# Optimization experiments

Hardware: AMD Instinct MI355X
Metric: run time of the kernel (lower is better)

The kernel has to match this reference:

```python
import jax, jax.numpy as jnp
import numpy as np

WAY, SHOT, P, FDIM, HDIM, NHEADS = 5, 5, 10, 640, 512, 8
H = W = 14
NUM_SPT = WAY * SHOT
EPS_BN = 1e-5
EPS_LN = 1e-5


def _l2norm(x, axis=-1):
    n = jnp.linalg.norm(x, axis=axis, keepdims=True)
    return x / jnp.maximum(n, 1e-12)


def _cbr(x, Wc, bc, g, beta):
    # 1x1 conv + BatchNorm(train stats) + ReLU. x: [N,C,H,W], Wc: [O,C]
    y = jnp.einsum('nchw,oc->nohw', x, Wc) + bc[None, :, None, None]
    mu = y.mean((0, 2, 3))
    var = y.var((0, 2, 3))
    y = (y - mu[None, :, None, None]) / jnp.sqrt(var[None, :, None, None] + EPS_BN)
    y = y * g[None, :, None, None] + beta[None, :, None, None]
    return jax.nn.relu(y)


def _mha(x, Wq, bq, Wk, bk, Wv, bv, Wa, ba, ln_g, ln_b):
    B, S, D = x.shape
    dk = D // NHEADS
    def proj(Wt, bt):
        return (x @ Wt.T + bt).reshape(B, S, NHEADS, dk).transpose(0, 2, 1, 3)
    q, k, v = proj(Wq, bq), proj(Wk, bk), proj(Wv, bv)
    scores = jnp.einsum('bhqd,bhkd->bhqk', q, k) / jnp.sqrt(jnp.asarray(dk, x.dtype))
    att = jax.nn.softmax(scores, axis=-1)
    ctx = jnp.einsum('bhqk,bhkd->bhqd', att, v).transpose(0, 2, 1, 3).reshape(B, S, D)
    out = ctx @ Wa.T + ba + x  # residual
    mu = out.mean(-1, keepdims=True)
    var = out.var(-1, keepdims=True)
    return ((out - mu) / jnp.sqrt(var + EPS_LN)) * ln_g + ln_b


def setup_inputs() -> dict:
    k = jax.random.key(0)
    ks = jax.random.split(k, 16)
    s = 0.02
    return {
        'key':   jax.random.normal(ks[0], (NUM_SPT + 75, FDIM, H, W), jnp.float32),
        'query': jax.random.normal(ks[1], (75, FDIM, H, W), jnp.float32),
        'Wc':  jax.random.normal(ks[2], (HDIM, FDIM), jnp.float32) * s,
        'bc':  jnp.zeros((HDIM,), jnp.float32),
        'g1':  jnp.ones((HDIM,), jnp.float32),
        'b1':  jnp.zeros((HDIM,), jnp.float32),
        'Wq':  jax.random.normal(ks[3], (HDIM, HDIM), jnp.float32) * s,
        'bq':  jnp.zeros((HDIM,), jnp.float32),
        'Wk':  jax.random.normal(ks[4], (HDIM, HDIM), jnp.float32) * s,
        'bk':  jnp.zeros((HDIM,), jnp.float32),
        'Wv':  jax.random.normal(ks[5], (HDIM, HDIM), jnp.float32) * s,
        'bv':  jnp.zeros((HDIM,), jnp.float32),
        'Wa':  jax.random.normal(ks[6], (HDIM, HDIM), jnp.float32) * s,
        'ba':  jnp.zeros((HDIM,), jnp.float32),
        'ln_g': jnp.ones((HDIM,), jnp.float32),
        'ln_b': jnp.zeros((HDIM,), jnp.float32),
        'Wm':  jax.random.normal(ks[7], (P, HDIM), jnp.float32) * s,
        'Wo':  jax.random.normal(ks[8], (FDIM, HDIM), jnp.float32) * s,
        'bo':  jnp.zeros((FDIM,), jnp.float32),
        'g2':  jnp.ones((FDIM,), jnp.float32),
        'b2':  jnp.zeros((FDIM,), jnp.float32),
    }


def reference(key, query, Wc, bc, g1, b1, Wq, bq, Wk, bk, Wv, bv, Wa, ba, ln_g, ln_b, Wm, Wo, bo, g2, b2):
    # proto_concept: conv1x1 + BN + ReLU
    key_ = _cbr(key, Wc, bc, g1, b1)                 # [B, HDIM, H, W]
    B, D, h, w = key_.shape
    feats = key_.transpose(0, 2, 3, 1).reshape(B, h * w, D)
    support = feats[:NUM_SPT].reshape(SHOT, WAY, h * w, D).mean(0)   # [WAY, hw, D]
    qf = feats[NUM_SPT:]                                             # [NQ, hw, D]
    nq = B - NUM_SPT

    support = _mha(support, Wq, bq, Wk, bk, Wv, bv, Wa, ba, ln_g, ln_b)
    qf = _mha(qf, Wq, bq, Wk, bk, Wv, bv, Wa, ba, ln_g, ln_b)

    # prototype formation: softmax over all support positions (dim 0)
    mw = (support @ Wm.T).reshape(-1, P, 1)          # [WAY*hw, P, 1]
    mw = jax.nn.softmax(mw, axis=0)
    sflat = support.reshape(-1, D)                   # [WAY*hw, D]
    protos = (mw * sflat[:, None, :]).sum(0)         # [P, D]

    # ---- query_loss (training branch) ----
    protos_n = _l2norm(protos)                       # [P, D]

    # diversity loss (faithful to original incl. triu over (P, D) dims)
    diff2 = (protos_n[None, :, :] - protos_n[:, None, :]) ** 2   # [P, P, D]
    dis = 1.0 - diff2[None]                                      # [1, P, P, D]
    dis = dis * (dis > 0).astype(dis.dtype)
    tri = jnp.triu(jnp.ones((P, D), dis.dtype), k=1)
    dis = dis * tri
    dis_loss = (dis.sum(1).sum(1) * 2.0 / (P * (P - 1))).mean()

    cst_loss = ((protos_n[1:] - protos_n[:-1]) ** 2).sum(-1).mean()

    # dual-softmax scoring (protos shared across batch)
    score = jnp.einsum('bnd,md->bnm', qf, protos_n)  # [NQ, hw, P]
    sp = jax.nn.softmax(score, axis=-1)
    new_q = _l2norm(jnp.einsum('bnm,md->bnd', sp, protos_n))

    idx = jnp.argmax(score, axis=-1)                 # top-1 proto per position
    pos = protos_n[idx]                              # [NQ, hw, D]
    fea_loss = jnp.mean((qf - pos) ** 2)

    uq = new_q.transpose(0, 2, 1).reshape(nq, D, h, w)
    updated = _cbr(uq, Wo, bo, g2, b2) + query       # [NQ, FDIM, H, W]
    return (updated, fea_loss, cst_loss, dis_loss)
```

## Files before the change

kernel.cpp:

```cpp
#include <hip/hip_runtime.h>
#include <math.h>

#define WAYS 5
#define SHOTS 5
#define PP 10
#define FDIMC 640
#define HD 512
#define SEQ 196
#define NB 100
#define NQB 75
#define NMHA 80
#define M1 (NB*SEQ)
#define MMHA (NMHA*SEQ)
#define MQ (NQB*SEQ)
#define NBLK_ROWK (MQ/4)
#define OUT_UPD (NQB*FDIMC*SEQ)

#define OFF_CS1S 0
#define OFF_CS1Q 512
#define OFF_CS2S 1024
#define OFF_CS2Q 1664
#define ZERO_FLOATS 2306
#define OFF_ST1SC 2308
#define OFF_ST1SH 2820
#define OFF_ST2SC 3332
#define OFF_ST2SH 3972
#define OFF_M    4612
#define OFF_PN   14412

#define RB 20480
#define RC (RB + 15439360)
#define RD (RC + 8028160)
#define RE (RD + 8028160)
#define RF (RE + 8028160)
#define RG (RF + 4014080)
#define RH (RG + 4014080)
#define OFF_XOUT (RB + 10000000)
#define OFF_FEAP (RF + 3763200)
#define OFF_WSM  RG
#define OFF_PPART (RG + 16384)

typedef __bf16 bf16x8 __attribute__((ext_vector_type(8)));
typedef float f32x4 __attribute__((ext_vector_type(4)));

__device__ __forceinline__ ushort f2bf(float f) {
  unsigned u = __float_as_uint(f);
  return (ushort)((u + 0x7fffu + ((u >> 16) & 1u)) >> 16);
}
__device__ __forceinline__ float bf2f(ushort u) {
  return __uint_as_float(((unsigned)u) << 16);
}

__device__ __forceinline__ f32x4 mfma16(bf16x8 a, bf16x8 b, f32x4 c) {
  return __builtin_amdgcn_mfma_f32_16x16x32_bf16(a, b, c, 0, 0, 0);
}

__device__ __forceinline__ float waveSum(float v) {
#pragma unroll
  for (int o = 32; o; o >>= 1) v += __shfl_xor(v, o, 64);
  return v;
}

__device__ __forceinline__ void gld16(const void* g, void* l) {
  __builtin_amdgcn_global_load_lds(
      (const __attribute__((address_space(1))) void*)g,
      (__attribute__((address_space(3))) void*)l,
      16, 0, 0);
}


__global__ __launch_bounds__(256) void key_transpose(const float* __restrict__ key,
                                                     ushort* __restrict__ keyT) {
  __shared__ float T[32][33];
  const int n = blockIdx.z, c0 = blockIdx.y*32, s0 = blockIdx.x*32;
  const int tj = threadIdx.x & 31, ti = threadIdx.x >> 5;
#pragma unroll
  for (int it = 0; it < 4; ++it) {
    const int cl = it*8 + ti;
    const int s = s0 + tj;
    T[cl][tj] = (s < SEQ) ? key[((size_t)n*FDIMC + c0 + cl)*SEQ + s] : 0.f;
  }
  __syncthreads();
#pragma unroll
  for (int it = 0; it < 4; ++it) {
    const int sl = it*8 + ti;
    const int s = s0 + sl;
    if (s < SEQ) keyT[((size_t)(n*SEQ + s))*FDIMC + c0 + tj] = f2bf(T[tj][sl]);
  }
}

__global__ void wconvert(const float* __restrict__ Wc, const float* __restrict__ Wq,
                         const float* __restrict__ Wk, const float* __restrict__ Wv,
                         const float* __restrict__ Wa, const float* __restrict__ Wo,
                         ushort* __restrict__ wh) {
  const int i = blockIdx.x*256 + threadIdx.x;
  float v;
  if (i < 327680) v = Wc[i];
  else if (i < 589824) v = Wq[i - 327680];
  else if (i < 851968) v = Wk[i - 589824];
  else if (i < 1114112) v = Wv[i - 851968];
  else if (i < 1376256) v = Wa[i - 1114112];
  else v = Wo[i - 1376256];
  wh[i] = f2bf(v);
}

template<int OM, int CS>
__global__ __launch_bounds__(256) void gemm_bf(const ushort* __restrict__ A,
    const ushort* __restrict__ W, const float* __restrict__ bias,
    float* __restrict__ Cf, ushort* __restrict__ Ch, int M, int N, int K,
    float* __restrict__ gsum, float* __restrict__ gsq) {
  __shared__ ushort As[128*32];
  __shared__ ushort Bs[128*32];
  __shared__ float csum[128], csq[128];
  const int tid = threadIdx.x;

  const int nwg = gridDim.x * gridDim.y;
  int flat = blockIdx.y * gridDim.x + blockIdx.x;
  {
    const int q = nwg >> 3, r = nwg & 7;
    const int j = flat & 7, t = flat >> 3;
    flat = (j < r ? j*(q+1) : r*(q+1) + (j-r)*q) + t;
  }
  const int m0 = (flat / gridDim.x) * 128;
  const int n0 = (flat % gridDim.x) * 128;

  const int w = tid >> 6, lane = tid & 63;
  const int wr = w >> 1, wc = w & 1;
  const int g = lane >> 4, c = lane & 15;

  const int srow = w*16 + (lane >> 2);
  const int sk   = (lane & 3) * 8;
  int ar0 = m0 + srow;       if (ar0 > M-1) ar0 = M-1;
  int ar1 = m0 + 64 + srow;  if (ar1 > M-1) ar1 = M-1;
  const ushort* Ap0 = A + (size_t)ar0*K + sk;
  const ushort* Ap1 = A + (size_t)ar1*K + sk;
  const ushort* Bp0 = W + (size_t)(n0 + srow)*K + sk;
  const ushort* Bp1 = W + (size_t)(n0 + 64 + srow)*K + sk;
  ushort* lA0 = &As[w*512];
  ushort* lA1 = &As[(4+w)*512];
  ushort* lB0 = &Bs[w*512];
  ushort* lB1 = &Bs[(4+w)*512];

  f32x4 acc[4][4];
#pragma unroll
  for (int i = 0; i < 4; ++i)
#pragma unroll
    for (int j = 0; j < 4; ++j) acc[i][j] = (f32x4)(0.0f);

  for (int k0 = 0; k0 < K; k0 += 32) {
    __syncthreads();
    gld16(Ap0 + k0, lA0);
    gld16(Ap1 + k0, lA1);
    gld16(Bp0 + k0, lB0);
    gld16(Bp1 + k0, lB1);
    __syncthreads();
    bf16x8 af[4], bfr[4];
#pragma unroll
    for (int mi = 0; mi < 4; ++mi)
      af[mi] = *(const bf16x8*)(&As[(wr*64 + mi*16 + c)*32 + g*8]);
#pragma unroll
    for (int ni = 0; ni < 4; ++ni)
      bfr[ni] = *(const bf16x8*)(&Bs[(wc*64 + ni*16 + c)*32 + g*8]);
#pragma unroll
    for (int mi = 0; mi < 4; ++mi)
#pragma unroll
      for (int ni = 0; ni < 4; ++ni)
        acc[mi][ni] = mfma16(af[mi], bfr[ni], acc[mi][ni]);
  }

  if (CS) {
    __syncthreads();
    if (tid < 128) { csum[tid] = 0.f; csq[tid] = 0.f; }
    __syncthreads();
  }

#pragma unroll
  for (int ni = 0; ni < 4; ++ni) {
    const int col = n0 + wc*64 + ni*16 + c;
    const float bb = bias[col];
    float ls = 0.f, lq = 0.f;
#pragma unroll
    for (int mi = 0; mi < 4; ++mi) {
#pragma unroll
      for (int q = 0; q < 4; ++q) {
        const int row = m0 + wr*64 + mi*16 + g*4 + q;
        if (row < M) {
          const float v = acc[mi][ni][q] + bb;
          if (OM == 0) Cf[(size_t)row*N + col] = v;
          else if (OM == 1) Ch[(size_t)row*N + col] = f2bf(v);
          else Ch[(size_t)row*N + col] = f2bf(v*0.125f);
          if (CS) { ls += v; lq += v*v; }
        }
      }
    }
    if (CS) {
      const int lcol = wc*64 + ni*16 + c;
      atomicAdd(&csum[lcol], ls);
      atomicAdd(&csq[lcol], lq);
    }
  }
  if (CS) {
    __syncthreads();
    if (tid < 128) {
      atomicAdd(&gsum[n0 + tid], csum[tid]);
      atomicAdd(&gsq[n0 + tid], csq[tid]);
    }
  }
}


__global__ void bn_finalize(const float* __restrict__ sums, const float* __restrict__ sumsq,
    const float* __restrict__ g, const float* __restrict__ b, int C, float invM,
    float* __restrict__ scale, float* __restrict__ shift) {
  const int c = blockIdx.x*256 + threadIdx.x;
  if (c >= C) return;
  const float mu = sums[c]*invM;
  const float var = sumsq[c]*invM - mu*mu;
  const float sc = rsqrtf(var + 1e-5f) * g[c];
  scale[c] = sc;
  shift[c] = b[c] - mu*sc;
}

__global__ __launch_bounds__(256) void bn1_apply(const ushort* __restrict__ y1,
    const float* __restrict__ scale, const float* __restrict__ shift,
    ushort* __restrict__ srawh, ushort* __restrict__ xbufh) {
  const int i8 = blockIdx.x*256 + threadIdx.x;
  if (i8 >= M1*HD/8) return;
  const int e = i8 << 3;
  const int col = e & (HD - 1);
  const uint4 raw = ((const uint4*)y1)[i8];
  unsigned rw[4] = {raw.x, raw.y, raw.z, raw.w};
  unsigned res[4];
#pragma unroll
  for (int j = 0; j < 4; ++j) {
    float v0 = bf2f((ushort)(rw[j] & 0xffffu));
    float v1 = bf2f((ushort)(rw[j] >> 16));
    v0 = fmaxf(fmaf(v0, scale[col + 2*j],     shift[col + 2*j]),     0.f);
    v1 = fmaxf(fmaf(v1, scale[col + 2*j + 1], shift[col + 2*j + 1]), 0.f);
    res[j] = (unsigned)f2bf(v0) | ((unsigned)f2bf(v1) << 16);
  }
  const uint4 o = make_uint4(res[0], res[1], res[2], res[3]);
  if (e < 25*SEQ*HD) ((uint4*)srawh)[i8] = o;
  else ((uint4*)xbufh)[i8 - (20*SEQ*HD/8)] = o;
}

__global__ void support_mean(const ushort* __restrict__ srawh, ushort* __restrict__ xbufh) {
  const int i8 = blockIdx.x*256 + threadIdx.x;
  if (i8 >= WAYS*SEQ*HD/8) return;
  const int e = i8 << 3;
  const int w = e / (SEQ*HD);
  const int rem = e - w*(SEQ*HD);
  float acc[8] = {};
#pragma unroll
  for (int s = 0; s < SHOTS; ++s) {
    const uint4 v = *(const uint4*)(srawh + (size_t)(s*WAYS + w)*(SEQ*HD) + rem);
    const unsigned rw[4] = {v.x, v.y, v.z, v.w};
#pragma unroll
    for (int j = 0; j < 4; ++j) {
      acc[2*j]   += bf2f((ushort)(rw[j] & 0xffffu));
      acc[2*j+1] += bf2f((ushort)(rw[j] >> 16));
    }
  }
  unsigned res[4];
#pragma unroll
  for (int j = 0; j < 4; ++j)
    res[j] = (unsigned)f2bf(acc[2*j]*0.2f) | ((unsigned)f2bf(acc[2*j+1]*0.2f) << 16);
  ((uint4*)xbufh)[i8] = make_uint4(res[0], res[1], res[2], res[3]);
}


__global__ __launch_bounds__(256) void attn_qk(const ushort* __restrict__ qb,
    const ushort* __restrict__ kb, ushort* __restrict__ P) {
  __shared__ ushort Ks[208*72];
  const int bh = blockIdx.x, b = bh >> 3, h = bh & 7;
  const int tid = threadIdx.x;
  for (int idx = tid; idx < 208*8; idx += 256) {
    const int row = idx >> 3, part = idx & 7;
    uint4 v = make_uint4(0u,0u,0u,0u);
    if (row < SEQ) v = *(const uint4*)(kb + ((size_t)(b*SEQ + row))*HD + h*64 + part*8);
    *(uint4*)(&Ks[row*72 + part*8]) = v;
  }
  __syncthreads();
  const int w = tid >> 6, lane = tid & 63, g = lane >> 4, c = lane & 15;
  for (int rt = w; rt < 13; rt += 4) {
    int qrow = b*SEQ + rt*16 + c; if (qrow > MMHA-1) qrow = MMHA-1;
    const bf16x8 aq0 = *(const bf16x8*)(qb + (size_t)qrow*HD + h*64 + g*8);
    const bf16x8 aq1 = *(const bf16x8*)(qb + (size_t)qrow*HD + h*64 + 32 + g*8);
    f32x4 acc[13];
#pragma unroll
    for (int ct = 0; ct < 13; ++ct) acc[ct] = (f32x4)(0.0f);
#pragma unroll
    for (int ct = 0; ct < 13; ++ct) {
      const bf16x8 b0 = *(const bf16x8*)(&Ks[(ct*16 + c)*72 + g*8]);
      const bf16x8 b1 = *(const bf16x8*)(&Ks[(ct*16 + c)*72 + 32 + g*8]);
      acc[ct] = mfma16(aq0, b0, acc[ct]);
      acc[ct] = mfma16(aq1, b1, acc[ct]);
    }
    if (c >= 4) acc[12] = (f32x4)(-1e30f);
    float mrow[4], Z[4];
#pragma unroll
    for (int q = 0; q < 4; ++q) {
      float mx = acc[0][q];
#pragma unroll
      for (int ct = 1; ct < 13; ++ct) mx = fmaxf(mx, acc[ct][q]);
      mrow[q] = mx;
    }
#pragma unroll
    for (int q = 0; q < 4; ++q) {
#pragma unroll
      for (int msk = 1; msk < 16; msk <<= 1)
        mrow[q] = fmaxf(mrow[q], __shfl_xor(mrow[q], msk, 64));
    }
#pragma unroll
    for (int q = 0; q < 4; ++q) Z[q] = 0.f;
#pragma unroll
    for (int ct = 0; ct < 13; ++ct)
#pragma unroll
      for (int q = 0; q < 4; ++q) {
        const float e = __expf(acc[ct][q] - mrow[q]);
        acc[ct][q] = e; Z[q] += e;
      }
#pragma unroll
    for (int q = 0; q < 4; ++q) {
#pragma unroll
      for (int msk = 1; msk < 16; msk <<= 1) Z[q] += __shfl_xor(Z[q], msk, 64);
      Z[q] = 1.f / Z[q];
    }
    const size_t pb = (size_t)bh*(208*232);
#pragma unroll
    for (int q = 0; q < 4; ++q) {
      ushort* pr = P + pb + (size_t)(rt*16 + g*4 + q)*232;
#pragma unroll
      for (int ct = 0; ct < 13; ++ct) pr[ct*16 + c] = f2bf(acc[ct][q]*Z[q]);
      pr[208 + c] = 0;
      if (c < 8) pr[224 + c] = 0;
    }
  }
}


__global__ __launch_bounds__(256) void v_transpose(const ushort* __restrict__ vb,
                                                   ushort* __restrict__ VT) {
  __shared__ ushort Vs[196*72];
  const int bh = blockIdx.x, b = bh >> 3, h = bh & 7;
  const int tid = threadIdx.x;
  for (int idx = tid; idx < 196*8; idx += 256) {
    const int row = idx >> 3, part = idx & 7;
    *(uint4*)(&Vs[row*72 + part*8]) =
        *(const uint4*)(vb + ((size_t)(b*SEQ + row))*HD + h*64 + part*8);
  }
  __syncthreads();
  ushort* o = VT + (size_t)bh*64*224;
  for (int idx = tid; idx < 64*224; idx += 256) {
    const int d = idx/224, s = idx - d*224;
    o[idx] = (s < SEQ) ? Vs[s*72 + d] : (ushort)0;
  }
}


__global__ __launch_bounds__(256) void attn_pv(const ushort* __restrict__ P,
    const ushort* __restrict__ VT, ushort* __restrict__ ctx) {
  __shared__ ushort Ps[112*232];
  const int bh = blockIdx.x, b = bh >> 3, h = bh & 7;
  const int tid = threadIdx.x, w = tid >> 6, lane = tid & 63, g = lane >> 4, c = lane & 15;
  bf16x8 bv[7];
  const ushort* vt = VT + (size_t)bh*64*224 + (size_t)(w*16 + c)*224;
#pragma unroll
  for (int ks = 0; ks < 7; ++ks) bv[ks] = *(const bf16x8*)(vt + ks*32 + g*8);
  const char* pg = (const char*)(P + (size_t)bh*(208*232));
#pragma unroll
  for (int half = 0; half < 2; ++half) {
    const int r0 = half ? 112 : 0;
    const int nbytes = half ? 96*464 : 112*464;
    __syncthreads();
    for (int byte = tid*16; byte < nbytes; byte += 4096)
      *(uint4*)((char*)Ps + byte) = *(const uint4*)(pg + r0*464 + byte);
    __syncthreads();
    const int rtlo = half ? 7 : 0, rthi = half ? 13 : 7;
    for (int rt = rtlo; rt < rthi; ++rt) {
      const int lrow = rt*16 - r0 + c;
      f32x4 acc = (f32x4)(0.0f);
#pragma unroll
      for (int ks = 0; ks < 7; ++ks) {
        const bf16x8 a = *(const bf16x8*)(&Ps[lrow*232 + ks*32 + g*8]);
        acc = mfma16(a, bv[ks], acc);
      }
#pragma unroll
      for (int q = 0; q < 4; ++q) {
        const int srow = rt*16 + g*4 + q;
        if (srow < SEQ)
          ctx[((size_t)(b*SEQ + srow))*HD + h*64 + w*16 + c] = f2bf(acc[q]);
      }
    }
  }
}


__global__ __launch_bounds__(256) void ln_kernel(const float* __restrict__ tmp,
    const ushort* __restrict__ xin, const float* __restrict__ g,
    const float* __restrict__ bta, ushort* __restrict__ outh) {
  const int row = blockIdx.x*4 + (threadIdx.x >> 6);
  const int lane = threadIdx.x & 63;
  const float* t = tmp + (size_t)row*HD;
  const ushort* x = xin + (size_t)row*HD;
  float v[8]; float s = 0.f;
#pragma unroll
  for (int i = 0; i < 8; ++i) {
    const float val = t[i*64 + lane] + bf2f(x[i*64 + lane]);
    v[i] = val; s += val;
  }
  s = waveSum(s);
  const float mu = s * (1.f/HD);
  float sq = 0.f;
#pragma unroll
  for (int i = 0; i < 8; ++i) { const float d = v[i] - mu; sq += d*d; }
  sq = waveSum(sq);
  const float istd = rsqrtf(sq*(1.f/HD) + 1e-5f);
#pragma unroll
  for (int i = 0; i < 8; ++i) {
    const int d = i*64 + lane;
    outh[(size_t)row*HD + d] = f2bf((v[i] - mu)*istd*g[d] + bta[d]);
  }
}


__global__ __launch_bounds__(256) void mw_kernel(const ushort* __restrict__ xout,
    const float* __restrict__ Wm, float* __restrict__ m) {
  const int row = blockIdx.x*4 + (threadIdx.x >> 6);
  const int lane = threadIdx.x & 63;
  const ushort* x = xout + (size_t)row*HD;
  float xv[8];
#pragma unroll
  for (int i = 0; i < 8; ++i) xv[i] = bf2f(x[i*64 + lane]);
#pragma unroll
  for (int p = 0; p < PP; ++p) {
    const float* wp = Wm + p*HD;
    float s = 0.f;
#pragma unroll
    for (int i = 0; i < 8; ++i) s = fmaf(xv[i], wp[i*64 + lane], s);
    s = waveSum(s);
    if (lane == 0) m[row*PP + p] = s;
  }
}

__global__ __launch_bounds__(256) void wsm_kernel(const float* __restrict__ m,
                                                  float* __restrict__ wsm) {
  __shared__ float red[256];
  const int p = blockIdx.x, tid = threadIdx.x;
  float lmax = -1e30f;
  for (int r = tid; r < 980; r += 256) lmax = fmaxf(lmax, m[r*PP + p]);
  red[tid] = lmax; __syncthreads();
  for (int s = 128; s; s >>= 1) { if (tid < s) red[tid] = fmaxf(red[tid], red[tid+s]); __syncthreads(); }
  const float bmax = red[0]; __syncthreads();
  float lsum = 0.f;
  for (int r = tid; r < 980; r += 256) {
    const float e = __expf(m[r*PP + p] - bmax);
    wsm[p*980 + r] = e; lsum += e;
  }
  red[tid] = lsum; __syncthreads();
  for (int s = 128; s; s >>= 1) { if (tid < s) red[tid] += red[tid+s]; __syncthreads(); }
  const float invZ = 1.f / red[0];
  for (int r = tid; r < 980; r += 256) wsm[p*980 + r] *= invZ;
}

__global__ __launch_bounds__(256) void protos_part(const float* __restrict__ wsm,
    const ushort* __restrict__ xout, float* __restrict__ part) {
  const int p = blockIdx.y, chunk = blockIdx.x, tid = threadIdx.x;
  const int r0 = chunk*49;
  float a0 = 0.f, a1 = 0.f;
  for (int r = r0; r < r0 + 49; ++r) {
    const float w = wsm[p*980 + r];
    a0 = fmaf(w, bf2f(xout[(size_t)r*HD + tid]), a0);
    a1 = fmaf(w, bf2f(xout[(size_t)r*HD + tid + 256]), a1);
  }
  float* o = part + (((size_t)p*20 + chunk) << 9);
  o[tid] = a0;
  o[tid + 256] = a1;
}

__global__ __launch_bounds__(256) void protos_fin(const float* __restrict__ part,
                                                  float* __restrict__ pn) {
  __shared__ float red[256];
  const int p = blockIdx.x, tid = threadIdx.x;
  float a0 = 0.f, a1 = 0.f;
  for (int cch = 0; cch < 20; ++cch) {
    const float* o = part + (((size_t)p*20 + cch) << 9);
    a0 += o[tid];
    a1 += o[tid + 256];
  }
  red[tid] = a0*a0 + a1*a1; __syncthreads();
  for (int s = 128; s; s >>= 1) { if (tid < s) red[tid] += red[tid+s]; __syncthreads(); }
  const float rn = 1.f / fmaxf(sqrtf(red[0]), 1e-12f);
  pn[p*HD + tid] = a0*rn;
  pn[p*HD + tid + 256] = a1*rn;
}

__global__ __launch_bounds__(256) void losses_kernel(const float* __restrict__ pn, float* __restrict__ out) {
  __shared__ float redc[256], redd[256];
  const int tid = threadIdx.x;
  float cpart = 0.f, dpart = 0.f;
  for (int d = tid; d < HD; d += 256) {
    float a[PP];
#pragma unroll
    for (int j = 0; j < PP; ++j) a[j] = pn[j*HD + d];
#pragma unroll
    for (int j = 0; j < PP; ++j) {
      if (d > j) {
#pragma unroll
        for (int i = 0; i < PP; ++i) {
          const float df = a[j] - a[i];
          const float t = 1.f - df*df;
          if (t > 0.f) dpart += t;
        }
      }
    }
#pragma unroll
    for (int j = 0; j < PP - 1; ++j) { const float df = a[j+1] - a[j]; cpart += df*df; }
  }
  redc[tid] = cpart; redd[tid] = dpart; __syncthreads();
  for (int s = 128; s; s >>= 1) {
    if (tid < s) { redc[tid] += redc[tid+s]; redd[tid] += redd[tid+s]; }
    __syncthreads();
  }
  if (tid == 0) {
    out[OUT_UPD + 1] = redc[0] / 9.f;
    out[OUT_UPD + 2] = redd[0] * (2.f / (90.f * 512.f));
  }
}

__global__ __launch_bounds__(256) void rowk(const ushort* __restrict__ xout, const float* __restrict__ pn,
    ushort* __restrict__ newq, float* __restrict__ feapart) {
  __shared__ float Ps[PP*HD];
  __shared__ float fred[4];
  const int tid = threadIdx.x;
  for (int idx = tid; idx < PP*HD; idx += 256) Ps[idx] = pn[idx];
  __syncthreads();
  const int row = blockIdx.x*4 + (tid >> 6);
  const int lane = tid & 63;
  const ushort* x = xout + (size_t)(WAYS*SEQ + row)*HD;
  float xv[8];
#pragma unroll
  for (int i = 0; i < 8; ++i) xv[i] = bf2f(x[i*64 + lane]);
  float sc[PP];
#pragma unroll
  for (int p = 0; p < PP; ++p) {
    float s = 0.f;
#pragma unroll
    for (int i = 0; i < 8; ++i) s = fmaf(xv[i], Ps[p*HD + i*64 + lane], s);
    sc[p] = waveSum(s);
  }
  float mx = sc[0]; int am = 0;
#pragma unroll
  for (int p = 1; p < PP; ++p) if (sc[p] > mx) { mx = sc[p]; am = p; }
  float Z = 0.f; float sp[PP];
#pragma unroll
  for (int p = 0; p < PP; ++p) { const float e = expf(sc[p] - mx); sp[p] = e; Z += e; }
  const float rz = 1.f / Z;
  float nv[8]; float ss = 0.f;
#pragma unroll
  for (int i = 0; i < 8; ++i) {
    float a = 0.f;
#pragma unroll
    for (int p = 0; p < PP; ++p) a = fmaf(sp[p], Ps[p*HD + i*64 + lane], a);
    a *= rz; nv[i] = a; ss += a*a;
  }
  ss = waveSum(ss);
  const float rn = 1.f / fmaxf(sqrtf(ss), 1e-12f);
#pragma unroll
  for (int i = 0; i < 8; ++i) newq[(size_t)row*HD + i*64 + lane] = f2bf(nv[i]*rn);
  float fp = 0.f;
#pragma unroll
  for (int i = 0; i < 8; ++i) { const float d = xv[i] - Ps[am*HD + i*64 + lane]; fp += d*d; }
  fp = waveSum(fp);
  if (lane == 0) fred[tid >> 6] = fp;
  __syncthreads();
  if (tid == 0) feapart[blockIdx.x] = fred[0] + fred[1] + fred[2] + fred[3];
}

__global__ __launch_bounds__(256) void fea_finalize(const float* __restrict__ feapart,
                                                    float* __restrict__ out) {
  __shared__ float red[256];
  float s = 0.f;
  for (int i = threadIdx.x; i < NBLK_ROWK; i += 256) s += feapart[i];
  red[threadIdx.x] = s; __syncthreads();
  for (int st = 128; st; st >>= 1) {
    if (threadIdx.x < st) red[threadIdx.x] += red[threadIdx.x + st];
    __syncthreads();
  }
  if (threadIdx.x == 0) out[OUT_UPD] = red[0] / (float)((size_t)NQB*SEQ*HD);
}

__global__ __launch_bounds__(256) void bn2_apply(const float* __restrict__ y2, const float* __restrict__ scale,
    const float* __restrict__ shift, const float* __restrict__ query, float* __restrict__ out) {
  __shared__ float tile[32][33];
  const int n = blockIdx.z, o0 = blockIdx.y*32, hw0 = blockIdx.x*32;
  const int tj = threadIdx.x & 31, ti = threadIdx.x >> 5;
#pragma unroll
  for (int it = 0; it < 4; ++it) {
    const int hw = hw0 + it*8 + ti;
    const int o = o0 + tj;
    float v = 0.f;
    if (hw < SEQ) v = fmaxf(fmaf(y2[((size_t)n*SEQ + hw)*FDIMC + o], scale[o], shift[o]), 0.f);
    tile[it*8 + ti][tj] = v;
  }
  __syncthreads();
#pragma unroll
  for (int it = 0; it < 4; ++it) {
    const int o = o0 + it*8 + ti;
    const int hw = hw0 + tj;
    if (hw < SEQ) {
      const size_t oi = ((size_t)n*FDIMC + o)*SEQ + hw;
      out[oi] = tile[tj][it*8 + ti] + query[oi];
    }
  }
}

extern "C" void kernel_launch(void* const* d_in, const int* in_sizes, int n_in,
                              void* d_out, int out_size, void* d_ws, size_t ws_size,
                              hipStream_t stream) {
  const float* key   = (const float*)d_in[0];
  const float* query = (const float*)d_in[1];
  const float* Wc    = (const float*)d_in[2];
  const float* bc    = (const float*)d_in[3];
  const float* g1    = (const float*)d_in[4];
  const float* b1    = (const float*)d_in[5];
  const float* Wq    = (const float*)d_in[6];
  const float* bq    = (const float*)d_in[7];
  const float* Wk    = (const float*)d_in[8];
  const float* bk    = (const float*)d_in[9];
  const float* Wv    = (const float*)d_in[10];
  const float* bv    = (const float*)d_in[11];
  const float* Wa    = (const float*)d_in[12];
  const float* ba    = (const float*)d_in[13];
  const float* ln_g  = (const float*)d_in[14];
  const float* ln_b  = (const float*)d_in[15];
  const float* Wm    = (const float*)d_in[16];
  const float* Wo    = (const float*)d_in[17];
  const float* bo    = (const float*)d_in[18];
  const float* g2    = (const float*)d_in[19];
  const float* b2    = (const float*)d_in[20];
  float* out = (float*)d_out;
  float* w = (float*)d_ws;

  ushort* y1h   = (ushort*)(w + RB);
  ushort* P     = (ushort*)(w + RB);
  float*  y2f   = w + RB;
  ushort* xouth = (ushort*)(w + OFF_XOUT);
  ushort* VT    = (ushort*)(w + RC);
  ushort* keyT  = (ushort*)(w + RD);
  ushort* qb    = (ushort*)(w + RD);
  float*  tmpf  = w + RD;
  ushort* xbufh = (ushort*)(w + RE);
  ushort* srawh = (ushort*)(w + RF);
  ushort* kb    = (ushort*)(w + RF);
  ushort* newq  = (ushort*)(w + RF);
  ushort* vb    = (ushort*)(w + RG);
  ushort* ctx   = (ushort*)(w + RG);
  ushort* wh    = (ushort*)(w + RH);
  float*  feapart = w + OFF_FEAP;
  float*  wsm   = w + OFF_WSM;
  float*  ppart = w + OFF_PPART;
  ushort* Wcb = wh;
  ushort* Wqb = wh + 327680;
  ushort* Wkb = wh + 589824;
  ushort* Wvb = wh + 851968;
  ushort* Wab = wh + 1114112;
  ushort* Wob = wh + 1376256;

  hipMemsetAsync(w, 0, ZERO_FLOATS*sizeof(float), stream);

  key_transpose<<<dim3(7, 20, NB), 256, 0, stream>>>(key, keyT);
  wconvert<<<6656, 256, 0, stream>>>(Wc, Wq, Wk, Wv, Wa, Wo, wh);

  gemm_bf<1,1><<<dim3(4, 154), 256, 0, stream>>>(keyT, Wcb, bc, nullptr, y1h, M1, HD, FDIMC,
                                                 w + OFF_CS1S, w + OFF_CS1Q);
  bn_finalize<<<2, 256, 0, stream>>>(w + OFF_CS1S, w + OFF_CS1Q, g1, b1, HD, 1.f/M1,
                                     w + OFF_ST1SC, w + OFF_ST1SH);
  bn1_apply<<<M1*HD/8/256, 256, 0, stream>>>(y1h, w + OFF_ST1SC, w + OFF_ST1SH, srawh, xbufh);
  support_mean<<<WAYS*SEQ*HD/8/256, 256, 0, stream>>>(srawh, xbufh);

  gemm_bf<2,0><<<dim3(4, 123), 256, 0, stream>>>(xbufh, Wqb, bq, nullptr, qb, MMHA, HD, HD, nullptr, nullptr);
  gemm_bf<1,0><<<dim3(4, 123), 256, 0, stream>>>(xbufh, Wkb, bk, nullptr, kb, MMHA, HD, HD, nullptr, nullptr);
  gemm_bf<1,0><<<dim3(4, 123), 256, 0, stream>>>(xbufh, Wvb, bv, nullptr, vb, MMHA, HD, HD, nullptr, nullptr);

  v_transpose<<<NMHA*8, 256, 0, stream>>>(vb, VT);
  attn_qk<<<NMHA*8, 256, 0, stream>>>(qb, kb, P);
  attn_pv<<<NMHA*8, 256, 0, stream>>>(P, VT, ctx);

  gemm_bf<0,0><<<dim3(4, 123), 256, 0, stream>>>(ctx, Wab, ba, tmpf, nullptr, MMHA, HD, HD, nullptr, nullptr);
  ln_kernel<<<MMHA/4, 256, 0, stream>>>(tmpf, xbufh, ln_g, ln_b, xouth);

  mw_kernel<<<245, 256, 0, stream>>>(xouth, Wm, w + OFF_M);
  wsm_kernel<<<PP, 256, 0, stream>>>(w + OFF_M, wsm);
  protos_part<<<dim3(20, PP), 256, 0, stream>>>(wsm, xouth, ppart);
  protos_fin<<<PP, 256, 0, stream>>>(ppart, w + OFF_PN);
  losses_kernel<<<1, 256, 0, stream>>>(w + OFF_PN, out);
  rowk<<<NBLK_ROWK, 256, 0, stream>>>(xouth, w + OFF_PN, newq, feapart);

  gemm_bf<0,1><<<dim3(5, 115), 256, 0, stream>>>(newq, Wob, bo, y2f, nullptr, MQ, FDIMC, HD,
                                                 w + OFF_CS2S, w + OFF_CS2Q);
  bn_finalize<<<3, 256, 0, stream>>>(w + OFF_CS2S, w + OFF_CS2Q, g2, b2, FDIMC, 1.f/MQ,
                                     w + OFF_ST2SC, w + OFF_ST2SH);
  fea_finalize<<<1, 256, 0, stream>>>(feapart, out);
  bn2_apply<<<dim3(7, 20, NQB), 256, 0, stream>>>(y2f, w + OFF_ST2SC, w + OFF_ST2SH, query, out);
}
```

Measured before the change: 370.4 us.

## Fuse QKV projections into one GEMM and double-buffer LDS with swizzle

Merges the three Q/K/V projection GEMMs into a single GEMM over concatenated weights (Wq, Wk, Wv are contiguous in the bf16 weight buffer) with a packed bias and a column-dependent 0.125 scale for the Q part. The attention kernels now read Q, K and V from one interleaved row-major buffer. The shared GEMM kernel gains double-buffered LDS tiles that prefetch the next K slice while computing, with one barrier per iteration and an XOR swizzle meant to reduce LDS bank conflicts. This saves two launches and improves load/compute overlap, at the cost of twice the LDS per block and a new workspace region.

```diff
diff --git a/kernel.cpp b/kernel.cpp
--- a/kernel.cpp
+++ b/kernel.cpp
@@ -6,6 +6,7 @@
 #define PP 10
 #define FDIMC 640
 #define HD 512
+#define QKVS 1536
 #define SEQ 196
 #define NB 100
 #define NQB 75
@@ -35,8 +36,10 @@
 #define RF (RE + 8028160)
 #define RG (RF + 4014080)
 #define RH (RG + 4014080)
+#define RQ 48424960
 #define OFF_XOUT (RB + 10000000)
 #define OFF_FEAP (RF + 3763200)
+#define OFF_BQKV (RF + 3767296)
 #define OFF_WSM  RG
 #define OFF_PPART (RG + 16384)
 
@@ -104,13 +107,20 @@
   wh[i] = f2bf(v);
 }
 
+__global__ void qkv_bias(const float* __restrict__ bq, const float* __restrict__ bk,
+                         const float* __restrict__ bv, float* __restrict__ o) {
+  const int i = blockIdx.x*256 + threadIdx.x;
+  if (i >= QKVS) return;
+  o[i] = (i < 512) ? bq[i] : (i < 1024 ? bk[i-512] : bv[i-1024]);
+}
+
 template<int OM, int CS>
 __global__ __launch_bounds__(256) void gemm_bf(const ushort* __restrict__ A,
     const ushort* __restrict__ W, const float* __restrict__ bias,
     float* __restrict__ Cf, ushort* __restrict__ Ch, int M, int N, int K,
     float* __restrict__ gsum, float* __restrict__ gsq) {
-  __shared__ ushort As[128*32];
-  __shared__ ushort Bs[128*32];
+  __shared__ ushort As[2][128*32];
+  __shared__ ushort Bs[2][128*32];
   __shared__ float csum[128], csq[128];
   const int tid = threadIdx.x;
 
@@ -118,8 +128,8 @@
   int flat = blockIdx.y * gridDim.x + blockIdx.x;
   {
     const int q = nwg >> 3, r = nwg & 7;
-    const int j = flat & 7, t = flat >> 3;
-    flat = (j < r ? j*(q+1) : r*(q+1) + (j-r)*q) + t;
+    const int j = flat & 7, tt = flat >> 3;
+    flat = (j < r ? j*(q+1) : r*(q+1) + (j-r)*q) + tt;
   }
   const int m0 = (flat / gridDim.x) * 128;
   const int n0 = (flat % gridDim.x) * 128;
@@ -129,17 +139,13 @@
   const int g = lane >> 4, c = lane & 15;
 
   const int srow = w*16 + (lane >> 2);
-  const int sk   = (lane & 3) * 8;
+  const int sk = ((lane & 3) ^ ((lane >> 2) & 3)) * 8;
   int ar0 = m0 + srow;       if (ar0 > M-1) ar0 = M-1;
   int ar1 = m0 + 64 + srow;  if (ar1 > M-1) ar1 = M-1;
   const ushort* Ap0 = A + (size_t)ar0*K + sk;
   const ushort* Ap1 = A + (size_t)ar1*K + sk;
   const ushort* Bp0 = W + (size_t)(n0 + srow)*K + sk;
   const ushort* Bp1 = W + (size_t)(n0 + 64 + srow)*K + sk;
-  ushort* lA0 = &As[w*512];
-  ushort* lA1 = &As[(4+w)*512];
-  ushort* lB0 = &Bs[w*512];
-  ushort* lB1 = &Bs[(4+w)*512];
 
   f32x4 acc[4][4];
 #pragma unroll
@@ -147,25 +153,43 @@
 #pragma unroll
     for (int j = 0; j < 4; ++j) acc[i][j] = (f32x4)(0.0f);
 
-  for (int k0 = 0; k0 < K; k0 += 32) {
-    __syncthreads();
-    gld16(Ap0 + k0, lA0);
-    gld16(Ap1 + k0, lA1);
-    gld16(Bp0 + k0, lB0);
-    gld16(Bp1 + k0, lB1);
-    __syncthreads();
+  const int nt = K >> 5;
+  gld16(Ap0, &As[0][w*512]);
+  gld16(Ap1, &As[0][(4+w)*512]);
+  gld16(Bp0, &Bs[0][w*512]);
+  gld16(Bp1, &Bs[0][(4+w)*512]);
+  asm volatile("s_waitcnt vmcnt(0)" ::: "memory");
+  __builtin_amdgcn_s_barrier();
+
+  int cur = 0;
+  for (int t = 0; t < nt; ++t) {
+    const int nxt = cur ^ 1;
+    if (t + 1 < nt) {
+      const int k0 = (t + 1) << 5;
+      gld16(Ap0 + k0, &As[nxt][w*512]);
+      gld16(Ap1 + k0, &As[nxt][(4+w)*512]);
+      gld16(Bp0 + k0, &Bs[nxt][w*512]);
+      gld16(Bp1 + k0, &Bs[nxt][(4+w)*512]);
+    }
     bf16x8 af[4], bfr[4];
 #pragma unroll
-    for (int mi = 0; mi < 4; ++mi)
-      af[mi] = *(const bf16x8*)(&As[(wr*64 + mi*16 + c)*32 + g*8]);
-#pragma unroll
-    for (int ni = 0; ni < 4; ++ni)
-      bfr[ni] = *(const bf16x8*)(&Bs[(wc*64 + ni*16 + c)*32 + g*8]);
+    for (int mi = 0; mi < 4; ++mi) {
+      const int row = wr*64 + mi*16 + c;
+      af[mi] = *(const bf16x8*)(&As[cur][row*32 + (g ^ (c & 3))*8]);
+    }
+#pragma unroll
+    for (int ni = 0; ni < 4; ++ni) {
+      const int row = wc*64 + ni*16 + c;
+      bfr[ni] = *(const bf16x8*)(&Bs[cur][row*32 + (g ^ (c & 3))*8]);
+    }
 #pragma unroll
     for (int mi = 0; mi < 4; ++mi)
 #pragma unroll
       for (int ni = 0; ni < 4; ++ni)
         acc[mi][ni] = mfma16(af[mi], bfr[ni], acc[mi][ni]);
+    asm volatile("s_waitcnt vmcnt(0)" ::: "memory");
+    __builtin_amdgcn_s_barrier();
+    cur = nxt;
   }
 
   if (CS) {
@@ -188,7 +212,7 @@
           const float v = acc[mi][ni][q] + bb;
           if (OM == 0) Cf[(size_t)row*N + col] = v;
           else if (OM == 1) Ch[(size_t)row*N + col] = f2bf(v);
-          else Ch[(size_t)row*N + col] = f2bf(v*0.125f);
+          else Ch[(size_t)row*N + col] = f2bf(col < HD ? v*0.125f : v);
           if (CS) { ls += v; lq += v*v; }
         }
       }
@@ -269,23 +293,24 @@
 }
 
 
-__global__ __launch_bounds__(256) void attn_qk(const ushort* __restrict__ qb,
-    const ushort* __restrict__ kb, ushort* __restrict__ P) {
+__global__ __launch_bounds__(256) void attn_qk(const ushort* __restrict__ qkv,
+                                               ushort* __restrict__ P) {
   __shared__ ushort Ks[208*72];
   const int bh = blockIdx.x, b = bh >> 3, h = bh & 7;
   const int tid = threadIdx.x;
   for (int idx = tid; idx < 208*8; idx += 256) {
     const int row = idx >> 3, part = idx & 7;
     uint4 v = make_uint4(0u,0u,0u,0u);
-    if (row < SEQ) v = *(const uint4*)(kb + ((size_t)(b*SEQ + row))*HD + h*64 + part*8);
+    if (row < SEQ)
+      v = *(const uint4*)(qkv + (size_t)(b*SEQ + row)*QKVS + 512 + h*64 + part*8);
     *(uint4*)(&Ks[row*72 + part*8]) = v;
   }
   __syncthreads();
   const int w = tid >> 6, lane = tid & 63, g = lane >> 4, c = lane & 15;
   for (int rt = w; rt < 13; rt += 4) {
     int qrow = b*SEQ + rt*16 + c; if (qrow > MMHA-1) qrow = MMHA-1;
-    const bf16x8 aq0 = *(const bf16x8*)(qb + (size_t)qrow*HD + h*64 + g*8);
-    const bf16x8 aq1 = *(const bf16x8*)(qb + (size_t)qrow*HD + h*64 + 32 + g*8);
+    const bf16x8 aq0 = *(const bf16x8*)(qkv + (size_t)qrow*QKVS + h*64 + g*8);
+    const bf16x8 aq1 = *(const bf16x8*)(qkv + (size_t)qrow*QKVS + h*64 + 32 + g*8);
     f32x4 acc[13];
 #pragma unroll
     for (int ct = 0; ct < 13; ++ct) acc[ct] = (f32x4)(0.0f);
@@ -339,7 +364,7 @@
 }
 
 
-__global__ __launch_bounds__(256) void v_transpose(const ushort* __restrict__ vb,
+__global__ __launch_bounds__(256) void v_transpose(const ushort* __restrict__ qkv,
                                                    ushort* __restrict__ VT) {
   __shared__ ushort Vs[196*72];
   const int bh = blockIdx.x, b = bh >> 3, h = bh & 7;
@@ -347,7 +372,7 @@
   for (int idx = tid; idx < 196*8; idx += 256) {
     const int row = idx >> 3, part = idx & 7;
     *(uint4*)(&Vs[row*72 + part*8]) =
-        *(const uint4*)(vb + ((size_t)(b*SEQ + row))*HD + h*64 + part*8);
+        *(const uint4*)(qkv + (size_t)(b*SEQ + row)*QKVS + 1024 + h*64 + part*8);
   }
   __syncthreads();
   ushort* o = VT + (size_t)bh*64*224;
@@ -648,22 +673,19 @@
   ushort* xouth = (ushort*)(w + OFF_XOUT);
   ushort* VT    = (ushort*)(w + RC);
   ushort* keyT  = (ushort*)(w + RD);
-  ushort* qb    = (ushort*)(w + RD);
   float*  tmpf  = w + RD;
   ushort* xbufh = (ushort*)(w + RE);
   ushort* srawh = (ushort*)(w + RF);
-  ushort* kb    = (ushort*)(w + RF);
   ushort* newq  = (ushort*)(w + RF);
-  ushort* vb    = (ushort*)(w + RG);
   ushort* ctx   = (ushort*)(w + RG);
   ushort* wh    = (ushort*)(w + RH);
+  ushort* qkv   = (ushort*)(w + RQ);
   float*  feapart = w + OFF_FEAP;
+  float*  bqkv  = w + OFF_BQKV;
   float*  wsm   = w + OFF_WSM;
   float*  ppart = w + OFF_PPART;
   ushort* Wcb = wh;
   ushort* Wqb = wh + 327680;
-  ushort* Wkb = wh + 589824;
-  ushort* Wvb = wh + 851968;
   ushort* Wab = wh + 1114112;
   ushort* Wob = wh + 1376256;
 
@@ -671,6 +693,7 @@
 
   key_transpose<<<dim3(7, 20, NB), 256, 0, stream>>>(key, keyT);
   wconvert<<<6656, 256, 0, stream>>>(Wc, Wq, Wk, Wv, Wa, Wo, wh);
+  qkv_bias<<<6, 256, 0, stream>>>(bq, bk, bv, bqkv);
 
   gemm_bf<1,1><<<dim3(4, 154), 256, 0, stream>>>(keyT, Wcb, bc, nullptr, y1h, M1, HD, FDIMC,
                                                  w + OFF_CS1S, w + OFF_CS1Q);
@@ -679,12 +702,11 @@
   bn1_apply<<<M1*HD/8/256, 256, 0, stream>>>(y1h, w + OFF_ST1SC, w + OFF_ST1SH, srawh, xbufh);
   support_mean<<<WAYS*SEQ*HD/8/256, 256, 0, stream>>>(srawh, xbufh);
 
-  gemm_bf<2,0><<<dim3(4, 123), 256, 0, stream>>>(xbufh, Wqb, bq, nullptr, qb, MMHA, HD, HD, nullptr, nullptr);
-  gemm_bf<1,0><<<dim3(4, 123), 256, 0, stream>>>(xbufh, Wkb, bk, nullptr, kb, MMHA, HD, HD, nullptr, nullptr);
-  gemm_bf<1,0><<<dim3(4, 123), 256, 0, stream>>>(xbufh, Wvb, bv, nullptr, vb, MMHA, HD, HD, nullptr, nullptr);
-
-  v_transpose<<<NMHA*8, 256, 0, stream>>>(vb, VT);
-  attn_qk<<<NMHA*8, 256, 0, stream>>>(qb, kb, P);
+  gemm_bf<3,0><<<dim3(12, 123), 256, 0, stream>>>(xbufh, Wqb, bqkv, nullptr, qkv,
+                                                  MMHA, QKVS, HD, nullptr, nullptr);
+
+  v_transpose<<<NMHA*8, 256, 0, stream>>>(qkv, VT);
+  attn_qk<<<NMHA*8, 256, 0, stream>>>(qkv, P);
   attn_pv<<<NMHA*8, 256, 0, stream>>>(P, VT, ctx);
 
   gemm_bf<0,0><<<dim3(4, 123), 256, 0, stream>>>(ctx, Wab, ba, tmpf, nullptr, MMHA, HD, HD, nullptr, nullptr);
```

After: 343.7 us. 7.2% less time.
